# Optimization experiments

Measured on AMD Instinct MI355X. Metric: run time of the kernel, lower is better.

Reference implementation:

```python
import jax, jax.numpy as jnp
import numpy as np

A = 0.5  # mixing coefficient `a` from __init__
B, S, C = 16, 4096, 512


def setup_inputs() -> dict:
    key = jax.random.key(0)
    k1, k2 = jax.random.split(key)
    predicted = jax.random.normal(k1, (B, S, C), dtype=jnp.float32)
    target = jax.random.randint(k2, (B, S), 0, C, dtype=jnp.int64)
    return {"predicted": predicted, "target": target}


def reference(predicted, target):
    # predicted: [B, S, C] logits, target: [B, S] int class ids.
    b, s, c = predicted.shape
    am = jnp.argmax(predicted, axis=-1)              # [B, S] per-position top-1 class (topk(1)[1])
    lse = jax.nn.logsumexp(predicted, axis=-1)       # [B, S]

    # counts[i, j, v] = #positions s with target[i,s]==j and argmax==v
    bidx = jnp.arange(b)[:, None]
    counts = jnp.zeros((b, c, c), dtype=jnp.int32).at[bidx, target, am].add(1)
    n = counts.sum(axis=-1)                          # [B, C] occurrences of class j in target[i]
    # torch.mode returns the smallest of the most common values; argmax over class value
    # returns the first (smallest) index achieving the max count, matching that tie-break.
    m = jnp.argmax(counts, axis=-1)                  # [B, C] mode label per (i, j)

    # pred_m[i, j, s] = predicted[i, s, m[i, j]]
    pred_m = predicted[jnp.arange(b)[:, None, None],
                       jnp.arange(s)[None, None, :],
                       m[:, :, None]]                # [B, C, S]
    # per-position CE against constant label m: lse - logit[m]
    term = lse[:, None, :] - pred_m                  # [B, C, S]

    maskT = target[:, None, :] == jnp.arange(c)[None, :, None]  # [B, C, S]
    eq_sum = jnp.sum(jnp.where(maskT, term, 0.0), axis=-1)      # [B, C]
    ne_sum = term.sum(axis=-1) - eq_sum                          # [B, C]

    nf = n.astype(predicted.dtype)
    present = n > 0
    eq_loss = eq_sum / jnp.maximum(nf, 1.0)
    ne_mean = ne_sum / jnp.maximum(s - nf, 1.0)
    ne_loss = 1.0 / jnp.where(present & (ne_mean != 0), ne_mean, 1.0)
    val = eq_loss * (1.0 - A) + A * ne_loss          # [B, C]

    keep = present & (val != 0)                      # cipherLoss[cipherLoss != 0]
    total = jnp.where(keep, val, 0.0).sum()
    cnt = jnp.maximum(keep.sum(), 1).astype(predicted.dtype)
    return total / cnt
```

## Files before the change

kernel.cpp:

```cpp
#include <hip/hip_runtime.h>
#include <cstdint>
#include <cstddef>

#define PB 16
#define PS 4096
#define PC 512

#define RPB 128
#define PANEL 32
#define NPANEL (PC / PANEL)
#define LSTRIDE 33

__global__ __launch_bounds__(256) void k0_init(int* __restrict__ nCnt,
                                               float* __restrict__ colsum,
                                               float* __restrict__ Lsum) {
    int i = blockIdx.x * 256 + threadIdx.x;
    if (i < PB * PC) { nCnt[i] = 0; colsum[i] = 0.0f; }
    if (i < PB) Lsum[i] = 0.0f;
}

__global__ __launch_bounds__(256) void k1_rows(const float* __restrict__ pred,
                                               const int* __restrict__ target,
                                               int* __restrict__ am,
                                               float* __restrict__ lse,
                                               int* __restrict__ nCnt,
                                               float* __restrict__ colsum,
                                               float* __restrict__ Lsum) {
    __shared__ float tile[2][RPB * LSTRIDE];
    __shared__ float colLDS[PC];

    const int t = threadIdx.x;
    const int rowBase = blockIdx.x * RPB;
    const int b = rowBase >> 12;
    const float* base = pred + (size_t)rowBase * PC;

    colLDS[t] = 0.0f; colLDS[t + 256] = 0.0f;

    const float* pj[4];
    int ldsOff[4];
    #pragma unroll
    for (int j = 0; j < 4; ++j) {
        int g = j * 256 + t;
        int r = g >> 3, c4 = g & 7;
        pj[j] = base + (size_t)r * PC + 4 * c4;
        ldsOff[j] = r * LSTRIDE + 4 * c4;
    }

    float4 reg[4];
    #pragma unroll
    for (int j = 0; j < 4; ++j) reg[j] = *(const float4*)(pj[j]);

    const int rt = t >> 1;
    const int h = t & 1;
    float mval = -3.4e38f;
    float ssum = 0.0f;
    int midx = 0;

    for (int p = 0; p < NPANEL; ++p) {
        float* tb = tile[p & 1];
        #pragma unroll
        for (int j = 0; j < 4; ++j) {
            float* d = tb + ldsOff[j];
            d[0] = reg[j].x; d[1] = reg[j].y; d[2] = reg[j].z; d[3] = reg[j].w;
        }
        __syncthreads();

        if (p + 1 < NPANEL) {
            #pragma unroll
            for (int j = 0; j < 4; ++j)
                reg[j] = *(const float4*)(pj[j] + (p + 1) * PANEL);
        }

        const int c0 = p * PANEL;
        const float* rowp = tb + rt * LSTRIDE + 16 * h;
        #pragma unroll
        for (int i = 0; i < 16; ++i) {
            float v = rowp[i];
            if (v > mval) {
                ssum = ssum * __expf(mval - v) + 1.0f;
                mval = v;
                midx = c0 + 16 * h + i;
            } else {
                ssum += __expf(v - mval);
            }
        }

        {
            int cl = t & 31, g2 = t >> 5;
            const float* colp = tb + (g2 * 16) * LSTRIDE + cl;
            float part = 0.0f;
            #pragma unroll
            for (int r = 0; r < 16; ++r) part += colp[r * LSTRIDE];
            atomicAdd(&colLDS[c0 + cl], part);
        }
    }

    float om = __shfl_xor(mval, 1, 64);
    float os = __shfl_xor(ssum, 1, 64);
    int   oi = __shfl_xor(midx, 1, 64);
    float M = fmaxf(mval, om);
    int IDX = (om > mval || (om == mval && oi < midx)) ? oi : midx;
    float S = ssum * __expf(mval - M) + os * __expf(om - M);
    float lse_v = M + __logf(S);

    if (h == 0) {
        int grow = rowBase + rt;
        lse[grow] = lse_v;
        am[grow] = IDX;
        int tg = target[grow];
        atomicAdd(&nCnt[(b << 9) + tg], 1);
    }

    float lv = (h == 0) ? lse_v : 0.0f;
    #pragma unroll
    for (int off = 1; off < 64; off <<= 1) lv += __shfl_xor(lv, off, 64);
    if ((t & 63) == 0) atomicAdd(&Lsum[b], lv);

    __syncthreads();
    atomicAdd(&colsum[(b << 9) + t], colLDS[t]);
    atomicAdd(&colsum[(b << 9) + t + 256], colLDS[t + 256]);
}

__global__ __launch_bounds__(512) void k23(const int* __restrict__ nCnt,
                                           const int* __restrict__ target,
                                           const int* __restrict__ am,
                                           int* __restrict__ offs,
                                           int* __restrict__ bucket,
                                           float* __restrict__ acc,
                                           int* __restrict__ done) {
    int b = blockIdx.x;
    int t = threadIdx.x;
    __shared__ int sc[PC];
    __shared__ int cur[PC];
    int x = nCnt[(b << 9) + t];
    sc[t] = x;
    __syncthreads();
    for (int off = 1; off < PC; off <<= 1) {
        int v = (t >= off) ? sc[t - off] : 0;
        __syncthreads();
        sc[t] += v;
        __syncthreads();
    }
    int g = (b << 12) + (sc[t] - x);
    offs[(b << 9) + t] = g;
    cur[t] = g;
    if (b == 0 && t < 3) {
        if (t < 2) acc[t] = 0.0f;
        else *done = 0;
    }
    __syncthreads();
    for (int i = t; i < PS; i += 512) {
        int gi = (b << 12) + i;
        int tg = target[gi];
        int a = am[gi];
        int pos = atomicAdd(&cur[tg], 1);
        bucket[pos] = i | (a << 12);
    }
}

__global__ __launch_bounds__(64) void k45(const float* __restrict__ pred,
                                          const int* __restrict__ nCnt,
                                          const int* __restrict__ offs,
                                          const int* __restrict__ bucket,
                                          const float* __restrict__ lse,
                                          const float* __restrict__ colsum,
                                          const float* __restrict__ Lsum,
                                          float* __restrict__ acc,
                                          int* __restrict__ done,
                                          float* __restrict__ out) {
    __shared__ int cache[64][33];
    int pair = blockIdx.x * 64 + threadIdx.x;
    int b = pair >> 9;
    int k = nCnt[pair];
    int start = offs[pair];

    float val = 0.0f;
    int keep = 0;

    if (k > 0) {
        int kc = (k < 32) ? k : 32;
        for (int i = 0; i < kc; ++i)
            cache[threadIdx.x][i] = bucket[start + i];

        int bc = 0, bvv = 0;
        if (k <= 32) {
            for (int i = 0; i < k; ++i) {
                int v = cache[threadIdx.x][i] >> 12;
                int c = 0;
                for (int j = 0; j < k; ++j) c += ((cache[threadIdx.x][j] >> 12) == v) ? 1 : 0;
                if (c > bc || (c == bc && v < bvv)) { bc = c; bvv = v; }
            }
        } else {
            for (int i = 0; i < k; ++i) {
                int v = bucket[start + i] >> 12;
                int c = 0;
                for (int j = 0; j < k; ++j)
                    c += ((bucket[start + j] >> 12) == v) ? 1 : 0;
                if (c > bc || (c == bc && v < bvv)) { bc = c; bvv = v; }
            }
        }
        int m = bvv;

        float lseSum = 0.0f, ep = 0.0f;
        for (int i = 0; i < k; ++i) {
            int e = (i < 32) ? cache[threadIdx.x][i] : bucket[start + i];
            int s = e & (PS - 1);
            lseSum += lse[(b << 12) + s];
            ep += pred[(((size_t)(b << 12)) + s) * PC + m];
        }
        float eq_sum = lseSum - ep;
        float total_term = Lsum[b] - colsum[(b << 9) + m];
        float ne_sum = total_term - eq_sum;
        float nf = (float)k;
        float eq_loss = eq_sum / fmaxf(nf, 1.0f);
        float ne_mean = ne_sum / fmaxf((float)PS - nf, 1.0f);
        float ne_loss = 1.0f / ((ne_mean != 0.0f) ? ne_mean : 1.0f);
        val = 0.5f * eq_loss + 0.5f * ne_loss;
        keep = (val != 0.0f) ? 1 : 0;
    }

    float vs = keep ? val : 0.0f;
    float ks = (float)keep;
    #pragma unroll
    for (int off = 1; off < 64; off <<= 1) {
        vs += __shfl_xor(vs, off, 64);
        ks += __shfl_xor(ks, off, 64);
    }
    if (threadIdx.x == 0) {
        atomicAdd(&acc[0], vs);
        atomicAdd(&acc[1], ks);
        __threadfence();
        int d = atomicAdd(done, 1);
        if (d == (int)gridDim.x - 1) {
            __threadfence();
            float a0 = atomicAdd(&acc[0], 0.0f);
            float a1 = atomicAdd(&acc[1], 0.0f);
            out[0] = a0 / fmaxf(a1, 1.0f);
        }
    }
}

extern "C" void kernel_launch(void* const* d_in, const int* in_sizes, int n_in,
                              void* d_out, int out_size, void* d_ws, size_t ws_size,
                              hipStream_t stream) {
    const float* pred = (const float*)d_in[0];
    const int* target = (const int*)d_in[1];
    float* out = (float*)d_out;

    char* w = (char*)d_ws;
    int*   am     = (int*)(w + 0);
    float* lse    = (float*)(w + 262144);
    int*   bucket = (int*)(w + 524288);
    int*   nCnt   = (int*)(w + 786432);
    int*   offs   = (int*)(w + 819200);
    float* colsum = (float*)(w + 851968);
    float* Lsum   = (float*)(w + 884736);
    float* acc    = (float*)(w + 884800);
    int*   done   = (int*)(w + 884808);

    k0_init<<<32, 256, 0, stream>>>(nCnt, colsum, Lsum);
    k1_rows<<<(PB * PS) / RPB, 256, 0, stream>>>(pred, target, am, lse, nCnt, colsum, Lsum);
    k23<<<PB, 512, 0, stream>>>(nCnt, target, am, offs, bucket, acc, done);
    k45<<<(PB * PC) / 64, 64, 0, stream>>>(pred, nCnt, offs, bucket, lse,
                                           colsum, Lsum, acc, done, out);
}
```

Baseline: 248.6 us.

## Remap row kernel to eight threads per row with wider panels and vector LDS

The row-statistics kernel now handles 32 rows per block over 64-column panels. Each row is split across 8 threads that read 8 values with two float4 LDS loads, take a panel-local max first, then accumulate the exps without branching. Per-row results are merged with a three-step shuffle reduction, LDS stores become float4, and launch bounds request higher occupancy. The aim is to shorten the serial online-softmax chain and cut divergence. In exchange there are four times as many blocks, and therefore four times as many global atomicAdds into colsum.

Measured after the change: 319.0 us. 1.28x slower.

```diff
diff --git a/kernel.cpp b/kernel.cpp
--- a/kernel.cpp
+++ b/kernel.cpp
@@ -6,10 +6,10 @@
 #define PS 4096
 #define PC 512
 
-#define RPB 128
-#define PANEL 32
+#define RPB 32
+#define PANEL 64
 #define NPANEL (PC / PANEL)
-#define LSTRIDE 33
+#define LSTRIDE 68
 
 __global__ __launch_bounds__(256) void k0_init(int* __restrict__ nCnt,
                                                float* __restrict__ colsum,
@@ -19,13 +19,13 @@
     if (i < PB) Lsum[i] = 0.0f;
 }
 
-__global__ __launch_bounds__(256) void k1_rows(const float* __restrict__ pred,
-                                               const int* __restrict__ target,
-                                               int* __restrict__ am,
-                                               float* __restrict__ lse,
-                                               int* __restrict__ nCnt,
-                                               float* __restrict__ colsum,
-                                               float* __restrict__ Lsum) {
+__global__ __launch_bounds__(256, 8) void k1_rows(const float* __restrict__ pred,
+                                                  const int* __restrict__ target,
+                                                  int* __restrict__ am,
+                                                  float* __restrict__ lse,
+                                                  int* __restrict__ nCnt,
+                                                  float* __restrict__ colsum,
+                                                  float* __restrict__ Lsum) {
     __shared__ float tile[2][RPB * LSTRIDE];
     __shared__ float colLDS[PC];
 
@@ -36,22 +36,22 @@
 
     colLDS[t] = 0.0f; colLDS[t + 256] = 0.0f;
 
-    const float* pj[4];
-    int ldsOff[4];
-    #pragma unroll
-    for (int j = 0; j < 4; ++j) {
+    const float* gp[2];
+    int ldsOff[2];
+    #pragma unroll
+    for (int j = 0; j < 2; ++j) {
         int g = j * 256 + t;
-        int r = g >> 3, c4 = g & 7;
-        pj[j] = base + (size_t)r * PC + 4 * c4;
+        int r = g >> 4, c4 = g & 15;
+        gp[j] = base + (size_t)r * PC + 4 * c4;
         ldsOff[j] = r * LSTRIDE + 4 * c4;
     }
 
-    float4 reg[4];
-    #pragma unroll
-    for (int j = 0; j < 4; ++j) reg[j] = *(const float4*)(pj[j]);
-
-    const int rt = t >> 1;
-    const int h = t & 1;
+    float4 reg[2];
+    #pragma unroll
+    for (int j = 0; j < 2; ++j) reg[j] = *(const float4*)(gp[j]);
+
+    const int rt = t >> 3;
+    const int h = t & 7;
     float mval = -3.4e38f;
     float ssum = 0.0f;
     int midx = 0;
@@ -59,54 +59,67 @@
     for (int p = 0; p < NPANEL; ++p) {
         float* tb = tile[p & 1];
         #pragma unroll
-        for (int j = 0; j < 4; ++j) {
+        for (int j = 0; j < 2; ++j) {
             float* d = tb + ldsOff[j];
-            d[0] = reg[j].x; d[1] = reg[j].y; d[2] = reg[j].z; d[3] = reg[j].w;
+            *(float4*)d = reg[j];
         }
         __syncthreads();
 
         if (p + 1 < NPANEL) {
             #pragma unroll
-            for (int j = 0; j < 4; ++j)
-                reg[j] = *(const float4*)(pj[j] + (p + 1) * PANEL);
-        }
-
-        const int c0 = p * PANEL;
-        const float* rowp = tb + rt * LSTRIDE + 16 * h;
-        #pragma unroll
-        for (int i = 0; i < 16; ++i) {
-            float v = rowp[i];
-            if (v > mval) {
-                ssum = ssum * __expf(mval - v) + 1.0f;
-                mval = v;
-                midx = c0 + 16 * h + i;
-            } else {
-                ssum += __expf(v - mval);
-            }
-        }
+            for (int j = 0; j < 2; ++j)
+                reg[j] = *(const float4*)(gp[j] + (p + 1) * PANEL);
+        }
+
+        const float* rowp = tb + rt * LSTRIDE + 8 * h;
+        float4 a = *(const float4*)(rowp);
+        float4 c = *(const float4*)(rowp + 4);
+        float v0=a.x, v1=a.y, v2=a.z, v3=a.w, v4=c.x, v5=c.y, v6=c.z, v7=c.w;
+
+        float pm = v0; int pi = 0;
+        if (v1 > pm) { pm = v1; pi = 1; }
+        if (v2 > pm) { pm = v2; pi = 2; }
+        if (v3 > pm) { pm = v3; pi = 3; }
+        if (v4 > pm) { pm = v4; pi = 4; }
+        if (v5 > pm) { pm = v5; pi = 5; }
+        if (v6 > pm) { pm = v6; pi = 6; }
+        if (v7 > pm) { pm = v7; pi = 7; }
+
+        if (pm > mval) {
+            ssum *= __expf(mval - pm);
+            mval = pm;
+            midx = p * PANEL + 8 * h + pi;
+        }
+        ssum += __expf(v0 - mval) + __expf(v1 - mval) + __expf(v2 - mval)
+              + __expf(v3 - mval) + __expf(v4 - mval) + __expf(v5 - mval)
+              + __expf(v6 - mval) + __expf(v7 - mval);
 
         {
-            int cl = t & 31, g2 = t >> 5;
-            const float* colp = tb + (g2 * 16) * LSTRIDE + cl;
+            int cl = t & 63, g2 = t >> 6;
+            const float* colp = tb + (8 * g2) * LSTRIDE + cl;
             float part = 0.0f;
             #pragma unroll
-            for (int r = 0; r < 16; ++r) part += colp[r * LSTRIDE];
-            atomicAdd(&colLDS[c0 + cl], part);
-        }
-    }
-
-    float om = __shfl_xor(mval, 1, 64);
-    float os = __shfl_xor(ssum, 1, 64);
-    int   oi = __shfl_xor(midx, 1, 64);
-    float M = fmaxf(mval, om);
-    int IDX = (om > mval || (om == mval && oi < midx)) ? oi : midx;
-    float S = ssum * __expf(mval - M) + os * __expf(om - M);
-    float lse_v = M + __logf(S);
+            for (int r = 0; r < 8; ++r) part += colp[r * LSTRIDE];
+            atomicAdd(&colLDS[p * PANEL + cl], part);
+        }
+    }
+
+    #pragma unroll
+    for (int off = 1; off < 8; off <<= 1) {
+        float om = __shfl_xor(mval, off, 64);
+        float os = __shfl_xor(ssum, off, 64);
+        int   oi = __shfl_xor(midx, off, 64);
+        float M = fmaxf(mval, om);
+        int nI = (om > mval || (om == mval && oi < midx)) ? oi : midx;
+        float nS = ssum * __expf(mval - M) + os * __expf(om - M);
+        mval = M; midx = nI; ssum = nS;
+    }
+    float lse_v = mval + __logf(ssum);
 
     if (h == 0) {
         int grow = rowBase + rt;
         lse[grow] = lse_v;
-        am[grow] = IDX;
+        am[grow] = midx;
         int tg = target[grow];
         atomicAdd(&nCnt[(b << 9) + tg], 1);
     }
```
